# Performance work log

Measured on AMD Instinct MI355X. Metric: run time of the kernel, lower is better.

Reference implementation:

```python
import jax, jax.numpy as jnp
from jax import lax
import numpy as np

B, C, H, W = 8, 256, 64, 64
DSTATE, DCONV, EXPAND = 16, 4, 2
DI = EXPAND * C          # 512 d_inner
DTR = (C + 15) // 16     # 16 dt_rank = ceil(d_model/16)

# ---------- helpers ----------

def _ln(x, g, b):
    m = x.mean(-1, keepdims=True)
    v = x.var(-1, keepdims=True)
    return (x - m) * lax.rsqrt(v + 1e-5) * g + b


def _bn(x, g, b):  # BatchNorm2d, training-mode batch stats
    m = x.mean((0, 2, 3), keepdims=True)
    v = x.var((0, 2, 3), keepdims=True)
    return (x - m) * lax.rsqrt(v + 1e-5) * g[None, :, None, None] + b[None, :, None, None]


def _gn(x, g, b, groups=32):
    Bb, Cc, Hh, Ww = x.shape
    xr = x.reshape(Bb, groups, Cc // groups, Hh, Ww)
    m = xr.mean((2, 3, 4), keepdims=True)
    v = xr.var((2, 3, 4), keepdims=True)
    xr = (xr - m) * lax.rsqrt(v + 1e-5)
    return xr.reshape(Bb, Cc, Hh, Ww) * g[None, :, None, None] + b[None, :, None, None]


def _hsig(x):  # h_sigmoid: relu6(x+3)/6
    return jnp.clip(x + 3.0, 0.0, 6.0) / 6.0


def _axial(v, idx, pos):
    # v: [B,C,N]; pos: [1,C,16] linearly resized to N (align_corners=False == half-pixel)
    N = v.shape[-1]
    pe = jax.image.resize(pos, (1, pos.shape[1], N), method='linear')
    return v + pe + idx  # idx interpolation is identity (same size)


def _dwconvT(x, w):
    # ConvTranspose2d(k=3, stride=2, pad=1, out_pad=1, groups=C) == lhs-dilated corr with flipped kernel
    wf = w[:, :, ::-1, ::-1]
    return lax.conv_general_dilated(x, wf, window_strides=(1, 1), padding=((1, 2), (1, 2)),
                                    lhs_dilation=(2, 2), dimension_numbers=('NCHW', 'OIHW', 'NCHW'),
                                    feature_group_count=x.shape[1])


def _mamba(h, in_w, conv_w, conv_b, xproj_w, dt_w, dt_b, Alog, Dp, out_w):
    # standard mamba_ssm Mamba block forward; h: [B,L,d_model]
    Bb, L, _ = h.shape
    di = in_w.shape[0] // 2
    N = Alog.shape[1]
    dtr = dt_w.shape[1]
    xz = h @ in_w.T                      # [B,L,2*di]
    xm, zg = xz[..., :di], xz[..., di:]
    # causal depthwise conv1d (pad K-1 left == torch pad both + slice [:L])
    xc = lax.conv_general_dilated(xm.transpose(0, 2, 1), conv_w, (1,), [(conv_w.shape[2] - 1, 0)],
                                  dimension_numbers=('NCH', 'OIH', 'NCH'), feature_group_count=di)
    u = jax.nn.silu(xc + conv_b[None, :, None]).transpose(0, 2, 1)  # [B,L,di]
    dbl = u @ xproj_w.T                  # [B,L,dtr+2N]
    dt = jax.nn.softplus(dbl[..., :dtr] @ dt_w.T + dt_b)            # [B,L,di]
    Bm = dbl[..., dtr:dtr + N]
    Cm = dbl[..., dtr + N:]
    A = -jnp.exp(Alog)                   # [di,N]
    dA = jnp.exp(dt[..., None] * A)      # [B,L,di,N]
    dBu = (dt * u)[..., None] * Bm[:, :, None, :]

    def step(hst, inp):
        dA_t, dBu_t = inp
        hst = dA_t * hst + dBu_t
        return hst, hst

    h0 = jnp.zeros((Bb, di, N), dt.dtype)
    _, hs = lax.scan(step, h0, (dA.transpose(1, 0, 2, 3), dBu.transpose(1, 0, 2, 3)))
    y = jnp.einsum('lbdn,bln->bld', hs, Cm) + Dp * u
    y = y * jax.nn.silu(zg)
    return y @ out_w.T


def _forward(x, pos_embed, ln_w, ln_b, proj_w, proj_b,
             up_dw_w, up_bn1_g, up_bn1_b, up_pw_w, up_bn2_g, up_bn2_b,
             down_pw_w, down_bn_g, down_bn_b, gn_g, gn_b,
             f_in_w, f_conv_w, f_conv_b, f_xproj_w, f_dt_w, f_dt_b, f_Alog, f_D, f_out_w,
             b_in_w, b_conv_w, b_conv_b, b_xproj_w, b_dt_w, b_dt_b, b_Alog, b_D, b_out_w):
    # upsample branch: dwconvT -> BN -> ReLU -> 1x1 -> BN -> ReLU6
    z = _dwconvT(x, up_dw_w)
    z = jax.nn.relu(_bn(z, up_bn1_g, up_bn1_b))
    z = jnp.einsum('oc,bchw->bohw', up_pw_w, z)
    z = jnp.clip(_bn(z, up_bn2_g, up_bn2_b), 0.0, 6.0)  # act1 = ReLU6
    dt = x.dtype
    col_max = _ln(_axial(x.max(2), jnp.argmax(x, 2).astype(dt), pos_embed).transpose(0, 2, 1), ln_w, ln_b)
    col_min = _ln(_axial(x.min(2), jnp.argmin(x, 2).astype(dt), pos_embed).transpose(0, 2, 1), ln_w, ln_b)
    row_max = _ln(_axial(x.max(3), jnp.argmax(x, 3).astype(dt), pos_embed).transpose(0, 2, 1), ln_w, ln_b)
    row_min = _ln(_axial(x.min(3), jnp.argmin(x, 3).astype(dt), pos_embed).transpose(0, 2, 1), ln_w, ln_b)
    result_max = jnp.concatenate([col_max, row_max], 1)  # [B, W+H, C]
    result_min = jnp.concatenate([col_min, row_min], 1)
    fpar = (f_in_w, f_conv_w, f_conv_b, f_xproj_w, f_dt_w, f_dt_b, f_Alog, f_D, f_out_w)
    bpar = (b_in_w, b_conv_w, b_conv_b, b_xproj_w, b_dt_w, b_dt_b, b_Alog, b_D, b_out_w)
    fmax = _ln(_mamba(result_max, *fpar), ln_w, ln_b)
    fmin = _ln(_mamba(result_min, *fpar), ln_w, ln_b)
    bmax = _ln(_mamba(jnp.flip(result_max, 1), *bpar), ln_w, ln_b)
    bmin = _ln(_mamba(jnp.flip(result_min, 1), *bpar), ln_w, ln_b)
    res_max = jnp.concatenate([fmax, jnp.flip(bmax, 1)], -1) @ proj_w.T + proj_b
    res_max = _ln(res_max, ln_w, ln_b)
    res_min = jnp.concatenate([fmin, jnp.flip(bmin, 1)], -1) @ proj_w.T + proj_b
    res_min = _ln(res_min, ln_w, ln_b)
    res = res_max[:, :, None, :] + res_min[:, None, :, :]  # [B,L,L,C], L=H+W
    res = res.transpose(0, 3, 1, 2)                        # [B,C,L,L] == [B,C,2H,2W]
    res = _hsig(res) * z
    res = _gn(res, gn_g, gn_b)
    res = jnp.einsum('oc,bchw->bohw', down_pw_w, res[:, :, ::2, ::2])  # 1x1 stride-2 conv
    res = _bn(res, down_bn_g, down_bn_b)
    res = _gn(res, gn_g, gn_b)
    res = res + x
    res = _gn(res, gn_g, gn_b)
    return res


def setup_inputs() -> dict:
    key = jax.random.key(0)
    ks = jax.random.split(key, 32)

    def n(i, shape, s=0.02):
        return jax.random.normal(ks[i], shape, jnp.float32) * s

    inp = {}
    inp['x'] = jax.random.normal(ks[0], (B, C, H, W), jnp.float32)
    inp['pos_embed'] = jax.random.normal(ks[1], (1, C, 16), jnp.float32)
    inp['ln_w'] = jnp.ones((C,), jnp.float32)
    inp['ln_b'] = jnp.zeros((C,), jnp.float32)
    inp['proj_w'] = n(2, (C, 2 * C))
    inp['proj_b'] = jnp.zeros((C,), jnp.float32)
    inp['up_dw_w'] = n(3, (C, 1, 3, 3), 0.1)
    inp['up_bn1_g'] = jnp.ones((C,), jnp.float32)
    inp['up_bn1_b'] = jnp.zeros((C,), jnp.float32)
    inp['up_pw_w'] = n(4, (C, C), 0.05)
    inp['up_bn2_g'] = jnp.ones((C,), jnp.float32)
    inp['up_bn2_b'] = jnp.zeros((C,), jnp.float32)
    inp['down_pw_w'] = n(5, (C, C), 0.05)
    inp['down_bn_g'] = jnp.ones((C,), jnp.float32)
    inp['down_bn_b'] = jnp.zeros((C,), jnp.float32)
    inp['gn_g'] = jnp.ones((C,), jnp.float32)
    inp['gn_b'] = jnp.zeros((C,), jnp.float32)
    Alog = jnp.tile(jnp.log(jnp.arange(1, DSTATE + 1, dtype=jnp.float32))[None, :], (DI, 1))
    dtb = jnp.full((DI,), float(np.log(np.expm1(0.01))), jnp.float32)
    for p, k0 in (('f', 6), ('b', 16)):
        inp[p + '_in_w'] = n(k0, (2 * DI, C))
        inp[p + '_conv_w'] = n(k0 + 1, (DI, 1, DCONV), 0.2)
        inp[p + '_conv_b'] = jnp.zeros((DI,), jnp.float32)
        inp[p + '_xproj_w'] = n(k0 + 2, (DTR + 2 * DSTATE, DI))
        inp[p + '_dt_w'] = n(k0 + 3, (DI, DTR), 0.1)
        inp[p + '_dt_b'] = dtb
        inp[p + '_Alog'] = Alog
        inp[p + '_D'] = jnp.ones((DI,), jnp.float32)
        inp[p + '_out_w'] = n(k0 + 4, (C, DI))
    return inp


def reference(x, pos_embed, ln_w, ln_b, proj_w, proj_b,
              up_dw_w, up_bn1_g, up_bn1_b, up_pw_w, up_bn2_g, up_bn2_b,
              down_pw_w, down_bn_g, down_bn_b, gn_g, gn_b,
              f_in_w, f_conv_w, f_conv_b, f_xproj_w, f_dt_w, f_dt_b, f_Alog, f_D, f_out_w,
              b_in_w, b_conv_w, b_conv_b, b_xproj_w, b_dt_w, b_dt_b, b_Alog, b_D, b_out_w):
    return _forward(x, pos_embed, ln_w, ln_b, proj_w, proj_b,
                    up_dw_w, up_bn1_g, up_bn1_b, up_pw_w, up_bn2_g, up_bn2_b,
                    down_pw_w, down_bn_g, down_bn_b, gn_g, gn_b,
                    f_in_w, f_conv_w, f_conv_b, f_xproj_w, f_dt_w, f_dt_b, f_Alog, f_D, f_out_w,
                    b_in_w, b_conv_w, b_conv_b, b_xproj_w, b_dt_w, b_dt_b, b_Alog, b_D, b_out_w)
```

## Files before the change

### kernel.cpp

```cpp
#include <hip/hip_runtime.h>
#include <hip/hip_bf16.h>

typedef __hip_bfloat16 bf16;
typedef __attribute__((ext_vector_type(8))) short bf16x8v;
typedef __attribute__((ext_vector_type(4))) short bf16x4v;
typedef __attribute__((ext_vector_type(4))) float f32x4v;

#define B_ 8
#define C_ 256
#define L_ 128
#define MB 1048576UL

__device__ inline float b2f(bf16 v){ return __bfloat162float(v); }
__device__ inline bf16 f2b(float v){ return __float2bfloat16(v); }
__device__ inline float siluf(float x){ return x / (1.f + expf(-x)); }
__device__ inline float softplusf(float x){ return (x > 20.f) ? x : log1pf(expf(x)); }
__device__ inline float vclamp(float v){ return fmaxf(v, 0.f) + 1e-5f; }

__device__ inline void bred2(float& a, float& b, float* red){
  int t = threadIdx.x;
  __syncthreads();
  red[t] = a; red[256 + t] = b;
  __syncthreads();
  for (int off = 128; off > 0; off >>= 1){
// ... 22 lines not shown
  if (tt <= 0.f) pe = pp[0];
  else if (tt >= 15.f) pe = pp[15];
  else { int f = (int)floorf(tt); float w = tt - (float)f; pe = pp[f]*(1.f - w) + pp[f+1]*w; }
  float vmax = -1e30f, vmin = 1e30f; int amax = 0, amin = 0;
  for (int j = 0; j < 64; j++){
    float v = xs[t][j];
    if (v > vmax){ vmax = v; amax = j; }
    if (v < vmin){ vmin = v; amin = j; }
  }
  long o = (long)(b*64 + t)*C_ + c;
  prowmax[o] = vmax + pe + (float)amax;
  prowmin[o] = vmin + pe + (float)amin;
  vmax = -1e30f; vmin = 1e30f; amax = 0; amin = 0;
  float sx = 0.f, sx2 = 0.f;
  for (int i = 0; i < 64; i++){
    float v = xs[i][t];
    if (v > vmax){ vmax = v; amax = i; }
    if (v < vmin){ vmin = v; amin = i; }
    sx += v; sx2 += v*v;
  }
  pcolmax[o] = vmax + pe + (float)amax;
  pcolmin[o] = vmin + pe + (float)amin;
  #pragma unroll
  for (int m = 1; m < 64; m <<= 1){ sx += __shfl_xor(sx, m); sx2 += __shfl_xor(sx2, m); }
  if (t == 0){ sxb[(b << 8) + c] = sx; sxb[2048 + (b << 8) + c] = sx2; }
}

__global__ __launch_bounds__(256) void pool2_kernel(const float* __restrict__ pcolmax, const float* __restrict__ pcolmin,
    const float* __restrict__ prowmax, const float* __restrict__ prowmin,
    const float* __restrict__ lnw, const float* __restrict__ lnb, bf16* __restrict__ hbuf)
{
  int r = blockIdx.x, b = blockIdx.y, c = threadIdx.x;
  __shared__ float red[512];
  int p = r & 63;
  long src = (long)(b*64 + p)*C_ + c;
  float vmax = (r < 64) ? pcolmax[src] : prowmax[src];
  float vmin = (r < 64) ? pcolmin[src] : prowmin[src];
  float gw = lnw[c], gb = lnb[c];
  long row = (long)b*L_ + r, frow = (long)b*L_ + (127 - r);
  float s = vmax, s2 = vmax*vmax;
  bred2(s, s2, red);
  float m = s*(1.f/256.f), var = s2*(1.f/256.f) - m*m;
  float o = (vmax - m)*rsqrtf(vclamp(var))*gw + gb;
  hbuf[0*262144 + row*C_ + c]  = f2b(o);
  hbuf[2*262144 + frow*C_ + c] = f2b(o);
  s = vmin; s2 = vmin*vmin;
  bred2(s, s2, red);
  m = s*(1.f/256.f); var = s2*(1.f/256.f) - m*m;
  o = (vmin - m)*rsqrtf(vclamp(var))*gw + gb;
  hbuf[1*262144 + row*C_ + c]  = f2b(o);
  hbuf[3*262144 + frow*C_ + c] = f2b(o);
}

__device__ inline float dwconvT_at(const float* __restrict__ xp, const float* __restrict__ w, int i, int j)
{
  float acc = 0.f;
  #pragma unroll
  for (int ki = 0; ki < 3; ki++){
    int pi = i + ki - 1;
    if (pi < 0 || (pi & 1)) continue;
    int xi = pi >> 1;
    if (xi >= 64) continue;
    #pragma unroll
    for (int kj = 0; kj < 3; kj++){
      int pj = j + kj - 1;
      if (pj < 0 || (pj & 1)) continue;
      int xj = pj >> 1;
      if (xj >= 64) continue;
      acc += w[(2-ki)*3 + (2-kj)] * xp[xi*64 + xj];
    }
  }
  return acc;
}

__global__ __launch_bounds__(256) void dwz1_kernel(const float* __restrict__ x, const float* __restrict__ dw,
    bf16* __restrict__ z1, float* __restrict__ bn1sum, float* __restrict__ bn1sq)
{
  int bc = blockIdx.x; int c = bc & 255;
  int tid = threadIdx.x;
  __shared__ float xs[4096];
  const float* xp = x + (long)bc*4096;
  for (int it = 0; it < 16; it++) xs[it*256 + tid] = xp[it*256 + tid];
  float w[9];
  #pragma unroll
  for (int q = 0; q < 9; q++) w[q] = dw[c*9 + q];
  __syncthreads();
  bf16* zp = z1 + (long)bc*16384;
  float s = 0.f, s2 = 0.f;
  for (int it = 0; it < 64; it++){
    int p = it*256 + tid; int i = p >> 7, j = p & 127;
    float acc = dwconvT_at(xs, w, i, j);
    zp[p] = f2b(acc);
    s += acc; s2 += acc*acc;
  }
  __shared__ float red[512];
  bred2(s, s2, red);
  if (tid == 0){ atomicAdd(&bn1sum[c], s); atomicAdd(&bn1sq[c], s2); }
}

__global__ void fin_bn_kernel(const float* __restrict__ sum, const float* __restrict__ sq,
                              const float* __restrict__ g, const float* __restrict__ b,
                              float cnt_inv, float* __restrict__ a, float* __restrict__ d)
{
  int c = threadIdx.x;
  float m = sum[c]*cnt_inv;
  float v = sq[c]*cnt_inv - m*m;
  float aa = g[c] * rsqrtf(vclamp(v));
  a[c] = aa;
  d[c] = b[c] - m*aa;
}

__global__ void fin_bn2_kernel(const float* __restrict__ part,
                               const float* __restrict__ g, const float* __restrict__ b,
                               float* __restrict__ a, float* __restrict__ d)
{
  int c = threadIdx.x;
  float s = 0.f, s2 = 0.f;
  for (int k = 0; k < 64; k++){ s += part[k*256 + c]; s2 += part[16384 + k*256 + c]; }
  float m = s*(1.f/131072.f);
  float v = s2*(1.f/131072.f) - m*m;
  float aa = g[c] * rsqrtf(vclamp(v));
  a[c] = aa;
  d[c] = b[c] - m*aa;
}

__global__ __launch_bounds__(256) void wcvt_all_kernel(
    const float* __restrict__ s0, const float* __restrict__ s1, const float* __restrict__ s2,
    const float* __restrict__ s3, const float* __restrict__ s4, const float* __restrict__ s5,
    const float* __restrict__ s6, const float* __restrict__ s7, const float* __restrict__ s8,
    bf16* __restrict__ d0, bf16* __restrict__ d1, bf16* __restrict__ d2,
    bf16* __restrict__ d3, bf16* __restrict__ d4, bf16* __restrict__ d5,
    bf16* __restrict__ d6, bf16* __restrict__ d7, bf16* __restrict__ d8)
{
  int seg = blockIdx.y;
  const float* s; bf16* d; int n;
  switch (seg){
    case 0: s = s0; d = d0; n = 262144; break;
    case 1: s = s1; d = d1; n = 262144; break;
    case 2: s = s2; d = d2; n = 24576;  break;
    case 3: s = s3; d = d3; n = 24576;  break;
    case 4: s = s4; d = d4; n = 131072; break;
    case 5: s = s5; d = d5; n = 131072; break;
    case 6: s = s6; d = d6; n = 131072; break;
    case 7: s = s7; d = d7; n = 65536;  break;
    default: s = s8; d = d8; n = 65536; break;
  }
  long i = ((long)blockIdx.x*256 + threadIdx.x)*4;
  if (i >= n) return;
  float4 v = *(const float4*)&s[i];
  bf16 o[4] = {f2b(v.x), f2b(v.y), f2b(v.z), f2b(v.w)};
  *(uint2*)&d[i] = *(const uint2*)o;
}

__global__ __launch_bounds__(256) void pwz_fused_kernel(const bf16* __restrict__ z1,
    const float* __restrict__ fa, const float* __restrict__ fd,
    const bf16* __restrict__ Wb, bf16* __restrict__ z2,
    float* __restrict__ bn2part)
{
  int b = blockIdx.y;
  int p0 = blockIdx.x*64;
  int tid = threadIdx.x;
  __shared__ __align__(16) short Tb[16384];
  {
    int pc = tid & 15, ch = tid >> 4;
    #pragma unroll
    for (int it = 0; it < 8; it++){
      int c2 = ch + it*16;
      int c = c2*2;
      const bf16* r0 = &z1[((long)(b*C_ + c))*16384 + p0 + pc*4];
      bf16x4v va = *(const bf16x4v*)r0;
      bf16x4v vb = *(const bf16x4v*)(r0 + 16384);
      float a0 = fa[c], d0 = fd[c], a1 = fa[c+1], d1 = fd[c+1];
      #pragma unroll
      for (int k = 0; k < 4; k++){
        int p = pc*4 + k;
        bf16 h0; *(short*)&h0 = va[k];
        bf16 h1; *(short*)&h1 = vb[k];
        bf16 o0 = f2b(fmaxf(b2f(h0)*a0 + d0, 0.f));
        bf16 o1 = f2b(fmaxf(b2f(h1)*a1 + d1, 0.f));
        unsigned int u = ((unsigned int)(*(unsigned short*)&o1) << 16) | (unsigned int)(*(unsigned short*)&o0);
        *(unsigned int*)((char*)Tb + tswz(p, c)) = u;
      }
    }
  }
  __syncthreads();
  int wave = tid >> 6, lane = tid & 63;
  int quad = lane >> 4, l16 = lane & 15;
  f32x4v acc[4][4];
  #pragma unroll
  for (int i = 0; i < 4; i++)
    #pragma unroll
    for (int j = 0; j < 4; j++) acc[i][j] = (f32x4v){0.f, 0.f, 0.f, 0.f};
  for (int k0 = 0; k0 < 256; k0 += 32){
    int c = k0 + quad*8;
    bf16x8v a[4], bb[4];
    #pragma unroll
    for (int ms = 0; ms < 4; ms++)
      a[ms] = *(const bf16x8v*)&Wb[(wave*64 + ms*16 + l16)*C_ + c];
    #pragma unroll
    for (int ns = 0; ns < 4; ns++){
      int p = ns*16 + l16;
      bb[ns] = *(const bf16x8v*)((const char*)Tb + tswz(p, c));
    }
    #pragma unroll
    for (int ms = 0; ms < 4; ms++)
      #pragma unroll
      for (int ns = 0; ns < 4; ns++)
        acc[ms][ns] = __builtin_amdgcn_mfma_f32_16x16x32_bf16(a[ms], bb[ns], acc[ms][ns], 0, 0, 0);
  }
  int slot = (blockIdx.x & 7) | (b << 3);
  #pragma unroll
  for (int ms = 0; ms < 4; ms++){
    int o = wave*64 + ms*16 + quad*4;
    #pragma unroll
    for (int r = 0; r < 4; r++){
      long rowbase = ((long)(b*C_ + o + r))*16384 + p0;
      float s = 0.f, s2 = 0.f;
      #pragma unroll
      for (int ns = 0; ns < 4; ns++){
        bf16 bv = f2b(acc[ms][ns][r]);
        z2[rowbase + ns*16 + l16] = bv;
        float vv = b2f(bv);
        s += vv; s2 += vv*vv;
      }
      #pragma unroll
      for (int m = 1; m < 16; m <<= 1){ s += __shfl_xor(s, m); s2 += __shfl_xor(s2, m); }
      if (l16 == 0){
        atomicAdd(&bn2part[slot*256 + o + r], s);
        atomicAdd(&bn2part[16384 + slot*256 + o + r], s2);
      }
    }
  }
}

__global__ __launch_bounds__(256) void inproj_mfma_kernel(const bf16* __restrict__ hb,
    const bf16* __restrict__ Wif, const bf16* __restrict__ Wib2, bf16* __restrict__ xz)
{
  int v = blockIdx.z;
  int m0 = blockIdx.y*256, n0 = blockIdx.x*64;
  const bf16* A = hb + (long)v*262144;
  const bf16* W = (v >= 2) ? Wib2 : Wif;
  bf16* out = xz + (long)v*1048576;
  int tid = threadIdx.x;
  int wave = tid >> 6, lane = tid & 63;
  int quad = lane >> 4, l16 = lane & 15;
  f32x4v acc[4][4];
  #pragma unroll
  for (int i = 0; i < 4; i++)
    #pragma unroll
    for (int j = 0; j < 4; j++) acc[i][j] = (f32x4v){0.f, 0.f, 0.f, 0.f};
  for (int k0 = 0; k0 < 256; k0 += 32){
    int c = k0 + quad*8;
    bf16x8v a[4], bb[4];
    #pragma unroll
    for (int ms = 0; ms < 4; ms++)
      a[ms] = *(const bf16x8v*)&A[(long)(m0 + wave*64 + ms*16 + l16)*256 + c];
    #pragma unroll
    for (int ns = 0; ns < 4; ns++)
      bb[ns] = *(const bf16x8v*)&W[(long)(n0 + ns*16 + l16)*256 + c];
    #pragma unroll
    for (int ms = 0; ms < 4; ms++)
      #pragma unroll
      for (int ns = 0; ns < 4; ns++)
        acc[ms][ns] = __builtin_amdgcn_mfma_f32_16x16x32_bf16(a[ms], bb[ns], acc[ms][ns], 0, 0, 0);
  }
  #pragma unroll
  for (int ms = 0; ms < 4; ms++){
    int m = m0 + wave*64 + ms*16 + quad*4;
    #pragma unroll
    for (int r = 0; r < 4; r++){
      long rowbase = (long)(m + r)*1024 + n0;
      #pragma unroll
      for (int ns = 0; ns < 4; ns++)
        out[rowbase + ns*16 + l16] = f2b(acc[ms][ns][r]);
    }
  }
}

__global__ __launch_bounds__(256) void xproj_mfma_kernel(const bf16* __restrict__ ub,
    const bf16* __restrict__ Wxf, const bf16* __restrict__ Wxb, float* __restrict__ dblb)
{
  int v = blockIdx.y;
  int m0 = blockIdx.x*256;
  const bf16* A = ub + (long)v*524288;
  const bf16* W = (v >= 2) ? Wxb : Wxf;
// ... 235 lines not shown
  float Dv = Dp[d];
  float h[4];
  #pragma unroll
  for (int n = 0; n < 4; n++) h[n] = 0.f;
  __syncthreads();
  bf16* yo = yb + (long)v*1024*512;
  for (int l = 0; l < 128; l++){
    float dtv = b2f(sdt[l*16 + dd]);
    float uv  = b2f(su [l*16 + dd]);
    float zgv = b2f(szg[l*16 + dd]);
    bf16x4v Bv = *(const bf16x4v*)&sbc[l*32 + qtr*4];
    bf16x4v Cv = *(const bf16x4v*)&sbc[l*32 + 16 + qtr*4];
    float dtu = dtv*uv;
    float acc = 0.f;
    #pragma unroll
    for (int n = 0; n < 4; n++){
      float dA = exp2f(dtv*a2[n]);
      bf16 tb; *(short*)&tb = Bv[n];
      bf16 tc; *(short*)&tc = Cv[n];
      h[n] = dA*h[n] + dtu*b2f(tb);
      acc += h[n]*b2f(tc);
    }
    acc += __shfl_xor(acc, 16);
    acc += __shfl_xor(acc, 32);
    if (qtr == 0)
      yo[(row + l)*512 + d] = f2b((acc + Dv*uv) * siluf(zgv));
  }
}

__global__ __launch_bounds__(256) void ln_kernel(const float* __restrict__ inb, bf16* __restrict__ outb0,
    bf16* __restrict__ outb1, float* __restrict__ outf,
    const float* __restrict__ lnw, const float* __restrict__ lnb, int mode)
{
  int r = blockIdx.x, b = blockIdx.y, v = blockIdx.z, c = threadIdx.x;
  long row = (long)b*L_ + r;
  float val = inb[((long)v*1024 + row)*C_ + c];
  __shared__ float red[512];
  float s = val, s2 = val*val;
  bred2(s, s2, red);
  float m = s*(1.f/256.f), var = s2*(1.f/256.f) - m*m;
  float o = (val - m)*rsqrtf(vclamp(var))*lnw[c] + lnb[c];
  if (mode == 1){
    long frow = (long)b*L_ + (127 - r);
    if (v == 0)      outb0[row*512 + c] = f2b(o);
    else if (v == 1) outb1[row*512 + c] = f2b(o);
    else if (v == 2) outb0[frow*512 + 256 + c] = f2b(o);
    else             outb1[frow*512 + 256 + c] = f2b(o);
  } else {
    outf[((long)v*1024 + row)*C_ + c] = o;
  }
}

__global__ __launch_bounds__(256) void hsig_kernel(bf16* __restrict__ z2, const float* __restrict__ rm,
    const float* __restrict__ rn, const float* __restrict__ a2, const float* __restrict__ d2,
    float* __restrict__ gnsum, float* __restrict__ gnsq)
{
  int c = blockIdx.x, b = blockIdx.y, tid = threadIdx.x;
  __shared__ float rms[128], rns[128];
  if (tid < 128){
    rms[tid] = rm[(long)(b*L_ + tid)*C_ + c];
    rns[tid] = rn[(long)(b*L_ + tid)*C_ + c];
  }
  __syncthreads();
  float aa = a2[c], dd = d2[c];
  bf16* zp = z2 + ((long)(b*C_ + c))*16384;
  float s = 0.f, s2 = 0.f;
  for (int g = 0; g < 16; g++){
    float tv[4]; int wq[4];
    #pragma unroll
    for (int q = 0; q < 4; q++){
      int p = g*1024 + q*256 + tid; int i = p >> 7, j = p & 127;
      float zv = b2f(zp[p])*aa + dd;
      zv = fminf(fmaxf(zv, 0.f), 6.f);
      float gate = rms[i] + rns[j];
      gate = fminf(fmaxf(gate + 3.f, 0.f), 6.f) * (1.f/6.f);
      float t = gate*zv;
      s += t; s2 += t*t;
      tv[q] = t;
      wq[q] = (((i | j) & 1) == 0) ? ((i >> 1)*64 + (j >> 1)) : -1;
    }
    __syncthreads();
    #pragma unroll
    for (int q = 0; q < 4; q++)
      if (wq[q] >= 0) zp[wq[q]] = f2b(tv[q]);
  }
  __shared__ float red[512];
  bred2(s, s2, red);
  if (tid == 0){ atomicAdd(&gnsum[b*32 + (c >> 3)], s); atomicAdd(&gnsq[b*32 + (c >> 3)], s2); }
}

__global__ void fin_gn_kernel(const float* __restrict__ gnsum, const float* __restrict__ gnsq,
                              const float* __restrict__ g, const float* __restrict__ bb,
                              float* __restrict__ gnA, float* __restrict__ gnD)
{
  int b = blockIdx.x, c = threadIdx.x, gr = c >> 3;
  float inv_cnt = 1.f/131072.f;
  float m = gnsum[b*32 + gr]*inv_cnt;
  float v = gnsq[b*32 + gr]*inv_cnt - m*m;
  float inv = rsqrtf(vclamp(v));
  float A = inv*g[c];
  gnA[b*C_ + c] = A;
  gnD[b*C_ + c] = bb[c] - m*A;
}

__global__ __launch_bounds__(256) void pwdown_fused_kernel(const bf16* __restrict__ z2,
    const float* __restrict__ gnA, const float* __restrict__ gnD,
    const bf16* __restrict__ Wb, const float* __restrict__ x,
    float* __restrict__ out, float* __restrict__ sds)
{
  int b = blockIdx.y;
  int p0 = blockIdx.x*64;
  int tid = threadIdx.x;
  __shared__ __align__(16) short Tb[16384];
  {
    int pc = tid & 15, ch = tid >> 4;
    #pragma unroll
    for (int it = 0; it < 8; it++){
      int c2 = ch + it*16;
      int c = c2*2;
      const bf16* r0 = &z2[((long)(b*C_ + c))*16384 + p0 + pc*4];
      bf16x4v va = *(const bf16x4v*)r0;
      bf16x4v vb = *(const bf16x4v*)(r0 + 16384);
      float a0 = gnA[b*C_ + c], d0 = gnD[b*C_ + c];
      float a1 = gnA[b*C_ + c + 1], d1 = gnD[b*C_ + c + 1];
      #pragma unroll
      for (int k = 0; k < 4; k++){
        int p = pc*4 + k;
        bf16 h0; *(short*)&h0 = va[k];
        bf16 h1; *(short*)&h1 = vb[k];
        bf16 o0 = f2b(b2f(h0)*a0 + d0);
        bf16 o1 = f2b(b2f(h1)*a1 + d1);
        unsigned int u = ((unsigned int)(*(unsigned short*)&o1) << 16) | (unsigned int)(*(unsigned short*)&o0);
        *(unsigned int*)((char*)Tb + tswz(p, c)) = u;
      }
    }
  }
  __syncthreads();
  int wave = tid >> 6, lane = tid & 63;
  int quad = lane >> 4, l16 = lane & 15;
  f32x4v acc[4][4];
  #pragma unroll
  for (int i = 0; i < 4; i++)
    #pragma unroll
    for (int j = 0; j < 4; j++) acc[i][j] = (f32x4v){0.f, 0.f, 0.f, 0.f};
  for (int k0 = 0; k0 < 256; k0 += 32){
    int c = k0 + quad*8;
    bf16x8v a[4], bb[4];
    #pragma unroll
    for (int ms = 0; ms < 4; ms++)
      a[ms] = *(const bf16x8v*)&Wb[(wave*64 + ms*16 + l16)*C_ + c];
    #pragma unroll
    for (int ns = 0; ns < 4; ns++){
      int p = ns*16 + l16;
      bb[ns] = *(const bf16x8v*)((const char*)Tb + tswz(p, c));
    }
    #pragma unroll
    for (int ms = 0; ms < 4; ms++)
      #pragma unroll
      for (int ns = 0; ns < 4; ns++)
        acc[ms][ns] = __builtin_amdgcn_mfma_f32_16x16x32_bf16(a[ms], bb[ns], acc[ms][ns], 0, 0, 0);
  }
  #pragma unroll
  for (int ms = 0; ms < 4; ms++){
    int o = wave*64 + ms*16 + quad*4;
    #pragma unroll
    for (int r = 0; r < 4; r++){
      long rowbase = ((long)(b*C_ + o + r))*4096 + p0;
      float sd = 0.f, sd2 = 0.f, sdx = 0.f;
      #pragma unroll
      for (int ns = 0; ns < 4; ns++){
        float v = acc[ms][ns][r];
        out[rowbase + ns*16 + l16] = v;
        float xv = x[rowbase + ns*16 + l16];
        sd += v; sd2 += v*v; sdx += v*xv;
      }
      #pragma unroll
      for (int m = 1; m < 16; m <<= 1){
        sd += __shfl_xor(sd, m); sd2 += __shfl_xor(sd2, m); sdx += __shfl_xor(sdx, m);
      }
      if (l16 == 0){
        int oc = (b << 8) + o + r;
        atomicAdd(&sds[oc], sd);
        atomicAdd(&sds[2048 + oc], sd2);
        atomicAdd(&sds[4096 + oc], sdx);
      }
    }
  }
}

__global__ void coeff_kernel(const float* __restrict__ sds, const float* __restrict__ sxb,
                             const float* __restrict__ dbn_g, const float* __restrict__ dbn_b,
                             const float* __restrict__ gn_g, const float* __restrict__ gn_b, float* __restrict__ pqr)
{
  int b = blockIdx.x, c = threadIdx.x, g = c >> 3;
  float sd = 0, sd2 = 0;
  for (int bb = 0; bb < 8; bb++){ sd += sds[bb*256 + c]; sd2 += sds[2048 + bb*256 + c]; }
  float inv_cnt = 1.f/32768.f;
  float mB = sd*inv_cnt;
  float vB = sd2*inv_cnt - mB*mB;
  float ab = dbn_g[c] * rsqrtf(vclamp(vB));
  float db = dbn_b[c] - mB*ab;
  float inv_n = 1.f/4096.f;
  float m = sds[b*256 + c]*inv_n, Ed2 = sds[2048 + b*256 + c]*inv_n;
  float mx = sxb[b*256 + c]*inv_n, Ex2 = sxb[2048 + b*256 + c]*inv_n;
  float Edx = sds[4096 + b*256 + c]*inv_n;
  float Ev = ab*m + db;
  float Ev2 = ab*ab*Ed2 + 2.f*ab*db*m + db*db;
  __shared__ float e1[256], e2[256];
  e1[c] = Ev; e2[c] = Ev2;
  __syncthreads();
  float m1 = 0, q1 = 0;
  for (int k = 0; k < 8; k++){ m1 += e1[(g << 3) + k]; q1 += e2[(g << 3) + k]; }
  m1 *= 0.125f; q1 *= 0.125f;
  float inv1 = rsqrtf(vclamp(q1 - m1*m1));
  float gg = gn_g[c];
  float A1 = inv1*gg;
  float D1 = gn_b[c] - m1*A1;
  float al = A1*ab;
  float be = A1*db + D1;
  float Et = al*m + be + mx;
  float Et2 = al*al*Ed2 + 2.f*al*be*m + be*be + 2.f*al*Edx + 2.f*be*mx + Ex2;
  __syncthreads();
  e1[c] = Et; e2[c] = Et2;
  __syncthreads();
  float m2 = 0, q2 = 0;
  for (int k = 0; k < 8; k++){ m2 += e1[(g << 3) + k]; q2 += e2[(g << 3) + k]; }
  m2 *= 0.125f; q2 *= 0.125f;
  float inv2 = rsqrtf(vclamp(q2 - m2*m2));
  float G = inv2*gg;
  float* o = pqr + (long)(b*C_ + c)*3;
  o[0] = G*al;
  o[1] = G;
  o[2] = G*(be - m2) + gn_b[c];
}

__global__ __launch_bounds__(256) void final_kernel(const float* __restrict__ x,
    const float* __restrict__ pqr, float* __restrict__ out)
{
  int c = blockIdx.x, b = blockIdx.y, tid = threadIdx.x;
  const float* o = pqr + (long)(b*C_ + c)*3;
  float P = o[0], Q = o[1], R = o[2];
  long base = ((long)(b*C_ + c))*4096;
  for (int it = 0; it < 16; it++){
    long idx = base + it*256 + tid;
    out[idx] = P*out[idx] + Q*x[idx] + R;
  }
}

extern "C" void kernel_launch(void* const* d_in, const int* in_sizes, int n_in,
                              void* d_out, int out_size, void* d_ws, size_t ws_size,
                              hipStream_t stream)
{
  (void)in_sizes; (void)n_in; (void)out_size; (void)ws_size;
  const float* x         = (const float*)d_in[0];
  const float* pos       = (const float*)d_in[1];
  const float* ln_w      = (const float*)d_in[2];
  const float* ln_b      = (const float*)d_in[3];
  const float* proj_w    = (const float*)d_in[4];
  const float* proj_b    = (const float*)d_in[5];
  const float* up_dw_w   = (const float*)d_in[6];
  const float* up_bn1_g  = (const float*)d_in[7];
  const float* up_bn1_b  = (const float*)d_in[8];
  const float* up_pw_w   = (const float*)d_in[9];
  const float* up_bn2_g  = (const float*)d_in[10];
  const float* up_bn2_b  = (const float*)d_in[11];
  const float* down_pw_w = (const float*)d_in[12];
  const float* down_bn_g = (const float*)d_in[13];
  const float* down_bn_b = (const float*)d_in[14];
  const float* gn_g      = (const float*)d_in[15];
  const float* gn_b      = (const float*)d_in[16];
  const float* f_in_w    = (const float*)d_in[17];
  const float* f_conv_w  = (const float*)d_in[18];
  const float* f_conv_b  = (const float*)d_in[19];
  const float* f_xproj_w = (const float*)d_in[20];
  const float* f_dt_w    = (const float*)d_in[21];
  const float* f_dt_b    = (const float*)d_in[22];
  const float* f_Alog    = (const float*)d_in[23];
  const float* f_D       = (const float*)d_in[24];
  const float* f_out_w   = (const float*)d_in[25];
  const float* b_in_w    = (const float*)d_in[26];
  const float* b_conv_w  = (const float*)d_in[27];
  const float* b_conv_b  = (const float*)d_in[28];
  const float* b_xproj_w = (const float*)d_in[29];
  const float* b_dt_w    = (const float*)d_in[30];
  const float* b_dt_b    = (const float*)d_in[31];
  const float* b_Alog    = (const float*)d_in[32];
  const float* b_D       = (const float*)d_in[33];
  const float* b_out_w   = (const float*)d_in[34];

  char* sb = (char*)d_ws;
  float* statz  = (float*)(sb);
  float* sds    = (float*)(sb + 6144);
  float* bn2part= (float*)(sb + 32768);
  float* abn    = (float*)(sb + 163840);
  float* gnAD   = (float*)(sb + 167936);
  float* sxb    = (float*)(sb + 184320);
  float* pqr    = (float*)(sb + 200704);
  float* rmrn  = (float*)(sb + 1*MB);
  bf16*  Wbbuf = (bf16*)(sb + 3*MB);
  bf16*  Wb2buf= (bf16*)(sb + 3*MB + 262144);
  bf16*  Wpb   = (bf16*)(sb + 3*MB + 524288);
  char* big = sb + 4*MB;
  float* pool4  = (float*)(big + 0*MB);
  bf16*  hbufb  = (bf16*)(big + 2*MB);
  bf16*  Wif    = (bf16*)(big + 4*MB);
  bf16*  Wib2   = (bf16*)(big + 4*MB + 524288);
  bf16*  Wxf    = (bf16*)(big + 5*MB);
  bf16*  Wxb    = (bf16*)(big + 5*MB + 65536);
  bf16*  Wof    = (bf16*)(big + 5*MB + 131072);
  bf16*  Wob    = (bf16*)(big + 5*MB + 393216);
  bf16*  xzbuf  = (bf16*)(big + 6*MB);
  bf16*  ubuf   = (bf16*)(big + 22*MB);
  float* dblbuf = (float*)(big + 30*MB);
  float* dtbuf  = (float*)(big + 31*MB);
  bf16*  ybuf   = (bf16*)(big + 39*MB);
  float* mout   = (float*)(big + 47*MB);
  bf16*  cbufb  = (bf16*)(big + 51*MB);
  float* respre = (float*)(big + 55*MB);
  bf16*  z1buf  = (bf16*)(big);
  bf16*  z2buf  = (bf16*)(big);
  float* dbuf   = (float*)d_out;

  float* bn1sum = statz;        float* bn1sq = statz + 256;
  float* gnsum  = statz + 1024; float* gnsq  = statz + 1280;
  float* abn1 = abn;       float* dbn1 = abn + 256;
  float* abn2 = abn + 512; float* dbn2 = abn + 768;
  float* gnA = gnAD;       float* gnD = gnAD + 2048;
  float* pcolmax = pool4;
  float* pcolmin = pool4 + 131072;
  float* prowmax = pool4 + 262144;
  float* prowmin = pool4 + 393216;

  hipMemsetAsync(statz, 0, 163840, stream);

  wcvt_all_kernel<<<dim3(256, 9), 256, 0, stream>>>(
      f_in_w, b_in_w, f_xproj_w, b_xproj_w, f_out_w, b_out_w, proj_w, up_pw_w, down_pw_w,
      Wif, Wib2, Wxf, Wxb, Wof, Wob, Wpb, Wbbuf, Wb2buf);

  pool1_kernel<<<dim3(256, 8), 64, 0, stream>>>(x, pos, pcolmax, pcolmin, prowmax, prowmin, sxb);
  pool2_kernel<<<dim3(128, 8), 256, 0, stream>>>(pcolmax, pcolmin, prowmax, prowmin, ln_w, ln_b, hbufb);
  inproj_mfma_kernel<<<dim3(16, 4, 4), 256, 0, stream>>>(hbufb, Wif, Wib2, xzbuf);
  conv1d_kernel<<<dim3(128, 8, 4), 512, 0, stream>>>(xzbuf, f_conv_w, f_conv_b, b_conv_w, b_conv_b, ubuf);
  xproj_mfma_kernel<<<dim3(4, 4), 256, 0, stream>>>(ubuf, Wxf, Wxb, dblbuf);
  gemm_kernel<<<dim3(8, 16, 4), 256, 0, stream>>>(dblbuf, 49152, 48, f_dt_w, b_dt_w, f_dt_b, b_dt_b, 2,
                                                  dtbuf, 524288, 512, 1024, 512, 16, 2);
  scan_kernel<<<dim3(32, 8, 4), 64, 0, stream>>>(dtbuf, ubuf, dblbuf, xzbuf, f_Alog, f_D, b_Alog, b_D, ybuf);
  outproj_mfma_kernel<<<dim3(4, 4, 4), 256, 0, stream>>>(ybuf, Wof, Wob, mout);
  ln_kernel<<<dim3(128, 8, 4), 256, 0, stream>>>(mout, cbufb, cbufb + 524288, nullptr, ln_w, ln_b, 1);
  pj_mfma_kernel<<<dim3(4, 4, 2), 256, 0, stream>>>(cbufb, Wpb, proj_b, respre);
  ln_kernel<<<dim3(128, 8, 2), 256, 0, stream>>>(respre, nullptr, nullptr, rmrn, ln_w, ln_b, 0);

  dwz1_kernel<<<2048, 256, 0, stream>>>(x, up_dw_w, z1buf, bn1sum, bn1sq);
  fin_bn_kernel<<<1, 256, 0, stream>>>(bn1sum, bn1sq, up_bn1_g, up_bn1_b, 1.f/131072.f, abn1, dbn1);
  pwz_fused_kernel<<<dim3(256, 8), 256, 0, stream>>>(z1buf, abn1, dbn1, Wbbuf, z2buf, bn2part);
  fin_bn2_kernel<<<1, 256, 0, stream>>>(bn2part, up_bn2_g, up_bn2_b, abn2, dbn2);

  hsig_kernel<<<dim3(256, 8), 256, 0, stream>>>(z2buf, rmrn, rmrn + 262144, abn2, dbn2, gnsum, gnsq);
  fin_gn_kernel<<<8, 256, 0, stream>>>(gnsum, gnsq, gn_g, gn_b, gnA, gnD);
  pwdown_fused_kernel<<<dim3(64, 8), 256, 0, stream>>>(z2buf, gnA, gnD, Wb2buf, x, dbuf, sds);
  coeff_kernel<<<8, 256, 0, stream>>>(sds, sxb, down_bn_g, down_bn_b, gn_g, gn_b, pqr);
  final_kernel<<<dim3(256, 8), 256, 0, stream>>>(x, pqr, (float*)d_out);
}
```

Measured before the change: 514.3 us.

## Fold stat-finalize kernels into consumers and prefetch second tile in pwz

Removes four tiny finalize launches (fin_bn, fin_bn2, fin_gn, coeff) by recomputing the BN/GN scale and shift inside the consuming kernels (pwz, hsig, pwdown, final). pwz_fused now handles two 64-pixel tiles per block, loading the second tile into registers while the first GEMM runs. The transposed depthwise conv is rewritten as a branch-free four-tap gather. This cuts launch and serialization overhead in exchange for redundant per-block statistics math and higher register and LDS use in pwz.

New measurement: 512.0 us. No clear change (-0.5%).

```diff
diff --git a/kernel.cpp b/kernel.cpp
--- a/kernel.cpp
+++ b/kernel.cpp
@@ -98,27 +98,6 @@
   hbuf[3*262144 + frow*C_ + c] = f2b(o);
 }
 
-__device__ inline float dwconvT_at(const float* __restrict__ xp, const float* __restrict__ w, int i, int j)
-{
-  float acc = 0.f;
-  #pragma unroll
-  for (int ki = 0; ki < 3; ki++){
-    int pi = i + ki - 1;
-    if (pi < 0 || (pi & 1)) continue;
-    int xi = pi >> 1;
-    if (xi >= 64) continue;
-    #pragma unroll
-    for (int kj = 0; kj < 3; kj++){
-      int pj = j + kj - 1;
-      if (pj < 0 || (pj & 1)) continue;
-      int xj = pj >> 1;
-      if (xj >= 64) continue;
-      acc += w[(2-ki)*3 + (2-kj)] * xp[xi*64 + xj];
-    }
-  }
-  return acc;
-}
-
 __global__ __launch_bounds__(256) void dwz1_kernel(const float* __restrict__ x, const float* __restrict__ dw,
     bf16* __restrict__ z1, float* __restrict__ bn1sum, float* __restrict__ bn1sq)
 {
@@ -135,39 +114,28 @@
   float s = 0.f, s2 = 0.f;
   for (int it = 0; it < 64; it++){
     int p = it*256 + tid; int i = p >> 7, j = p & 127;
-    float acc = dwconvT_at(xs, w, i, j);
+    int xi = i >> 1, xj = j >> 1;
+    int io = i & 1, jo = j & 1;
+    int xi1 = (xi < 63) ? xi + 1 : 63;
+    int xj1 = (xj < 63) ? xj + 1 : 63;
+    float XA = xs[xi*64 + xj];
+    float XB = xs[xi*64 + xj1];
+    float XC = xs[xi1*64 + xj];
+    float XD = xs[xi1*64 + xj1];
+    float wA = jo ? (io ? w[8] : w[5]) : (io ? w[7] : w[4]);
+    float wB = (jo && j < 127) ? (io ? w[6] : w[3]) : 0.f;
+    float wC = (io && i < 127) ? (jo ? w[2] : w[1]) : 0.f;
+    float wD = (io && jo && i < 127 && j < 127) ? w[0] : 0.f;
+    float acc = wA*XA;
+    acc += wB*XB;
+    acc += wC*XC;
+    acc += wD*XD;
     zp[p] = f2b(acc);
     s += acc; s2 += acc*acc;
   }
   __shared__ float red[512];
   bred2(s, s2, red);
   if (tid == 0){ atomicAdd(&bn1sum[c], s); atomicAdd(&bn1sq[c], s2); }
-}
-
-__global__ void fin_bn_kernel(const float* __restrict__ sum, const float* __restrict__ sq,
-                              const float* __restrict__ g, const float* __restrict__ b,
-                              float cnt_inv, float* __restrict__ a, float* __restrict__ d)
-{
-  int c = threadIdx.x;
-  float m = sum[c]*cnt_inv;
-  float v = sq[c]*cnt_inv - m*m;
-  float aa = g[c] * rsqrtf(vclamp(v));
-  a[c] = aa;
-  d[c] = b[c] - m*aa;
-}
-
-__global__ void fin_bn2_kernel(const float* __restrict__ part,
-                               const float* __restrict__ g, const float* __restrict__ b,
-                               float* __restrict__ a, float* __restrict__ d)
-{
-  int c = threadIdx.x;
-  float s = 0.f, s2 = 0.f;
-  for (int k = 0; k < 64; k++){ s += part[k*256 + c]; s2 += part[16384 + k*256 + c]; }
-  float m = s*(1.f/131072.f);
-  float v = s2*(1.f/131072.f) - m*m;
-  float aa = g[c] * rsqrtf(vclamp(v));
-  a[c] = aa;
-  d[c] = b[c] - m*aa;
 }
 
 __global__ __launch_bounds__(256) void wcvt_all_kernel(
@@ -198,38 +166,10 @@
   *(uint2*)&d[i] = *(const uint2*)o;
 }
 
-__global__ __launch_bounds__(256) void pwz_fused_kernel(const bf16* __restrict__ z1,
-    const float* __restrict__ fa, const float* __restrict__ fd,
-    const bf16* __restrict__ Wb, bf16* __restrict__ z2,
-    float* __restrict__ bn2part)
-{
-  int b = blockIdx.y;
-  int p0 = blockIdx.x*64;
-  int tid = threadIdx.x;
-  __shared__ __align__(16) short Tb[16384];
-  {
-    int pc = tid & 15, ch = tid >> 4;
-    #pragma unroll
-    for (int it = 0; it < 8; it++){
-      int c2 = ch + it*16;
-      int c = c2*2;
-      const bf16* r0 = &z1[((long)(b*C_ + c))*16384 + p0 + pc*4];
-      bf16x4v va = *(const bf16x4v*)r0;
-      bf16x4v vb = *(const bf16x4v*)(r0 + 16384);
-      float a0 = fa[c], d0 = fd[c], a1 = fa[c+1], d1 = fd[c+1];
-      #pragma unroll
-      for (int k = 0; k < 4; k++){
-        int p = pc*4 + k;
-        bf16 h0; *(short*)&h0 = va[k];
-        bf16 h1; *(short*)&h1 = vb[k];
-        bf16 o0 = f2b(fmaxf(b2f(h0)*a0 + d0, 0.f));
-        bf16 o1 = f2b(fmaxf(b2f(h1)*a1 + d1, 0.f));
-        unsigned int u = ((unsigned int)(*(unsigned short*)&o1) << 16) | (unsigned int)(*(unsigned short*)&o0);
-        *(unsigned int*)((char*)Tb + tswz(p, c)) = u;
-      }
-    }
-  }
-  __syncthreads();
+__device__ inline void pwz_gemm_tile(const short* __restrict__ Tbh, const bf16* __restrict__ Wb,
+    bf16* __restrict__ z2, float* __restrict__ bn2part,
+    int b, int pbase, int slot, int tid)
+{
   int wave = tid >> 6, lane = tid & 63;
   int quad = lane >> 4, l16 = lane & 15;
   f32x4v acc[4][4];
@@ -246,7 +186,7 @@
     #pragma unroll
     for (int ns = 0; ns < 4; ns++){
       int p = ns*16 + l16;
-      bb[ns] = *(const bf16x8v*)((const char*)Tb + tswz(p, c));
+      bb[ns] = *(const bf16x8v*)((const char*)Tbh + tswz(p, c));
     }
     #pragma unroll
     for (int ms = 0; ms < 4; ms++)
@@ -254,13 +194,12 @@
       for (int ns = 0; ns < 4; ns++)
         acc[ms][ns] = __builtin_amdgcn_mfma_f32_16x16x32_bf16(a[ms], bb[ns], acc[ms][ns], 0, 0, 0);
   }
-  int slot = (blockIdx.x & 7) | (b << 3);
   #pragma unroll
   for (int ms = 0; ms < 4; ms++){
     int o = wave*64 + ms*16 + quad*4;
     #pragma unroll
     for (int r = 0; r < 4; r++){
-      long rowbase = ((long)(b*C_ + o + r))*16384 + p0;
+      long rowbase = ((long)(b*C_ + o + r))*16384 + pbase;
       float s = 0.f, s2 = 0.f;
       #pragma unroll
       for (int ns = 0; ns < 4; ns++){
@@ -277,6 +216,73 @@
       }
     }
   }
+}
+
+__global__ __launch_bounds__(256) void pwz_fused_kernel(const bf16* __restrict__ z1,
+    const float* __restrict__ bn1sum, const float* __restrict__ bn1sq,
+    const float* __restrict__ g1, const float* __restrict__ b1,
+    const bf16* __restrict__ Wb, bf16* __restrict__ z2,
+    float* __restrict__ bn2part)
+{
+  int b = blockIdx.y;
+  int p0 = blockIdx.x*128;
+  int tid = threadIdx.x;
+  __shared__ __align__(16) short Tb[2][16384];
+  __shared__ float aa[256], dd[256];
+  {
+    float m = bn1sum[tid]*(1.f/131072.f);
+    float v = bn1sq[tid]*(1.f/131072.f) - m*m;
+    float a = g1[tid]*rsqrtf(vclamp(v));
+    aa[tid] = a; dd[tid] = b1[tid] - m*a;
+  }
+  __syncthreads();
+  int pc = tid & 15, ch = tid >> 4;
+  #pragma unroll
+  for (int it = 0; it < 8; it++){
+    int c = (ch + it*16)*2;
+    const bf16* r0 = &z1[((long)(b*C_ + c))*16384 + p0 + pc*4];
+    bf16x4v va = *(const bf16x4v*)r0;
+    bf16x4v vb = *(const bf16x4v*)(r0 + 16384);
+    float a0 = aa[c], d0 = dd[c], a1 = aa[c+1], d1 = dd[c+1];
+    #pragma unroll
+    for (int k = 0; k < 4; k++){
+      int p = pc*4 + k;
+      bf16 h0; *(short*)&h0 = va[k];
+      bf16 h1; *(short*)&h1 = vb[k];
+      bf16 o0 = f2b(fmaxf(b2f(h0)*a0 + d0, 0.f));
+      bf16 o1 = f2b(fmaxf(b2f(h1)*a1 + d1, 0.f));
+      unsigned int u = ((unsigned int)(*(unsigned short*)&o1) << 16) | (unsigned int)(*(unsigned short*)&o0);
+      *(unsigned int*)((char*)&Tb[0][0] + tswz(p, c)) = u;
+    }
+  }
+  bf16x4v t1a[8], t1b[8];
+  #pragma unroll
+  for (int it = 0; it < 8; it++){
+    int c = (ch + it*16)*2;
+    const bf16* r1 = &z1[((long)(b*C_ + c))*16384 + p0 + 64 + pc*4];
+    t1a[it] = *(const bf16x4v*)r1;
+    t1b[it] = *(const bf16x4v*)(r1 + 16384);
+  }
+  __syncthreads();
+  int slot = (blockIdx.x & 7) | (b << 3);
+  pwz_gemm_tile(&Tb[0][0], Wb, z2, bn2part, b, p0, slot, tid);
+  #pragma unroll
+  for (int it = 0; it < 8; it++){
+    int c = (ch + it*16)*2;
+    float a0 = aa[c], d0 = dd[c], a1 = aa[c+1], d1 = dd[c+1];
+    #pragma unroll
+    for (int k = 0; k < 4; k++){
+      int p = pc*4 + k;
+      bf16 h0; *(short*)&h0 = t1a[it][k];
+      bf16 h1; *(short*)&h1 = t1b[it][k];
+      bf16 o0 = f2b(fmaxf(b2f(h0)*a0 + d0, 0.f));
+      bf16 o1 = f2b(fmaxf(b2f(h1)*a1 + d1, 0.f));
+      unsigned int u = ((unsigned int)(*(unsigned short*)&o1) << 16) | (unsigned int)(*(unsigned short*)&o0);
+      *(unsigned int*)((char*)&Tb[1][0] + tswz(p, c)) = u;
+    }
+  }
+  __syncthreads();
+  pwz_gemm_tile(&Tb[1][0], Wb, z2, bn2part, b, p0 + 64, slot, tid);
 }
 
 __global__ __launch_bounds__(256) void inproj_mfma_kernel(const bf16* __restrict__ hb,
@@ -618,17 +624,25 @@
 }
 
 __global__ __launch_bounds__(256) void hsig_kernel(bf16* __restrict__ z2, const float* __restrict__ rm,
-    const float* __restrict__ rn, const float* __restrict__ a2, const float* __restrict__ d2,
+    const float* __restrict__ rn, const float* __restrict__ bn2part,
+    const float* __restrict__ g2, const float* __restrict__ b2,
     float* __restrict__ gnsum, float* __restrict__ gnsq)
 {
   int c = blockIdx.x, b = blockIdx.y, tid = threadIdx.x;
+  __shared__ float red[512];
+  float pa = 0.f, pb = 0.f;
+  if (tid < 64){ pa = bn2part[tid*256 + c]; pb = bn2part[16384 + tid*256 + c]; }
+  bred2(pa, pb, red);
+  float mm2 = pa*(1.f/131072.f);
+  float vv2 = pb*(1.f/131072.f) - mm2*mm2;
+  float aa = g2[c] * rsqrtf(vclamp(vv2));
+  float dd = b2[c] - mm2*aa;
   __shared__ float rms[128], rns[128];
   if (tid < 128){
     rms[tid] = rm[(long)(b*L_ + tid)*C_ + c];
     rns[tid] = rn[(long)(b*L_ + tid)*C_ + c];
   }
   __syncthreads();
-  float aa = a2[c], dd = d2[c];
   bf16* zp = z2 + ((long)(b*C_ + c))*16384;
   float s = 0.f, s2 = 0.f;
   for (int g = 0; g < 16; g++){
@@ -650,27 +664,13 @@
     for (int q = 0; q < 4; q++)
       if (wq[q] >= 0) zp[wq[q]] = f2b(tv[q]);
   }
-  __shared__ float red[512];
   bred2(s, s2, red);
   if (tid == 0){ atomicAdd(&gnsum[b*32 + (c >> 3)], s); atomicAdd(&gnsq[b*32 + (c >> 3)], s2); }
 }
 
-__global__ void fin_gn_kernel(const float* __restrict__ gnsum, const float* __restrict__ gnsq,
-                              const float* __restrict__ g, const float* __restrict__ bb,
-                              float* __restrict__ gnA, float* __restrict__ gnD)
-{
-  int b = blockIdx.x, c = threadIdx.x, gr = c >> 3;
-  float inv_cnt = 1.f/131072.f;
-  float m = gnsum[b*32 + gr]*inv_cnt;
-  float v = gnsq[b*32 + gr]*inv_cnt - m*m;
-  float inv = rsqrtf(vclamp(v));
-  float A = inv*g[c];
-  gnA[b*C_ + c] = A;
-  gnD[b*C_ + c] = bb[c] - m*A;
-}
-
 __global__ __launch_bounds__(256) void pwdown_fused_kernel(const bf16* __restrict__ z2,
-    const float* __restrict__ gnA, const float* __restrict__ gnD,
+    const float* __restrict__ gnsum, const float* __restrict__ gnsq,
+    const float* __restrict__ gn_g, const float* __restrict__ gn_b,
     const bf16* __restrict__ Wb, const float* __restrict__ x,
     float* __restrict__ out, float* __restrict__ sds)
 {
@@ -678,6 +678,14 @@
   int p0 = blockIdx.x*64;
   int tid = threadIdx.x;
   __shared__ __align__(16) short Tb[16384];
+  __shared__ float gA[256], gD[256];
+  {
+    float m = gnsum[b*32 + (tid >> 3)]*(1.f/131072.f);
+    float v = gnsq[b*32 + (tid >> 3)]*(1.f/131072.f) - m*m;
+    float A = rsqrtf(vclamp(v))*gn_g[tid];
+    gA[tid] = A; gD[tid] = gn_b[tid] - m*A;
+  }
+  __syncthreads();
   {
     int pc = tid & 15, ch = tid >> 4;
     #pragma unroll
@@ -687,8 +695,8 @@
       const bf16* r0 = &z2[((long)(b*C_ + c))*16384 + p0 + pc*4];
       bf16x4v va = *(const bf16x4v*)r0;
       bf16x4v vb = *(const bf16x4v*)(r0 + 16384);
-      float a0 = gnA[b*C_ + c], d0 = gnD[b*C_ + c];
-      float a1 = gnA[b*C_ + c + 1], d1 = gnD[b*C_ + c + 1];
+      float a0 = gA[c], d0 = gD[c];
+      float a1 = gA[c + 1], d1 = gD[c + 1];
       #pragma unroll
       for (int k = 0; k < 4; k++){
         int p = pc*4 + k;
@@ -754,58 +762,57 @@
   }
 }
 
-__global__ void coeff_kernel(const float* __restrict__ sds, const float* __restrict__ sxb,
-                             const float* __restrict__ dbn_g, const float* __restrict__ dbn_b,
-                             const float* __restrict__ gn_g, const float* __restrict__ gn_b, float* __restrict__ pqr)
-{
-  int b = blockIdx.x, c = threadIdx.x, g = c >> 3;
-  float sd = 0, sd2 = 0;
-  for (int bb = 0; bb < 8; bb++){ sd += sds[bb*256 + c]; sd2 += sds[2048 + bb*256 + c]; }
-  float inv_cnt = 1.f/32768.f;
-  float mB = sd*inv_cnt;
-  float vB = sd2*inv_cnt - mB*mB;
-  float ab = dbn_g[c] * rsqrtf(vclamp(vB));
-  float db = dbn_b[c] - mB*ab;
-  float inv_n = 1.f/4096.f;
-  float m = sds[b*256 + c]*inv_n, Ed2 = sds[2048 + b*256 + c]*inv_n;
-  float mx = sxb[b*256 + c]*inv_n, Ex2 = sxb[2048 + b*256 + c]*inv_n;
-  float Edx = sds[4096 + b*256 + c]*inv_n;
-  float Ev = ab*m + db;
-  float Ev2 = ab*ab*Ed2 + 2.f*ab*db*m + db*db;
-  __shared__ float e1[256], e2[256];
-  e1[c] = Ev; e2[c] = Ev2;
-  __syncthreads();
-  float m1 = 0, q1 = 0;
-  for (int k = 0; k < 8; k++){ m1 += e1[(g << 3) + k]; q1 += e2[(g << 3) + k]; }
-  m1 *= 0.125f; q1 *= 0.125f;
-  float inv1 = rsqrtf(vclamp(q1 - m1*m1));
-  float gg = gn_g[c];
-  float A1 = inv1*gg;
-  float D1 = gn_b[c] - m1*A1;
-  float al = A1*ab;
-  float be = A1*db + D1;
-  float Et = al*m + be + mx;
-  float Et2 = al*al*Ed2 + 2.f*al*be*m + be*be + 2.f*al*Edx + 2.f*be*mx + Ex2;
-  __syncthreads();
-  e1[c] = Et; e2[c] = Et2;
-  __syncthreads();
-  float m2 = 0, q2 = 0;
-  for (int k = 0; k < 8; k++){ m2 += e1[(g << 3) + k]; q2 += e2[(g << 3) + k]; }
+__global__ __launch_bounds__(256) void final_kernel(const float* __restrict__ x,
+    const float* __restrict__ sds, const float* __restrict__ sxb,
+    const float* __restrict__ dbn_g, const float* __restrict__ dbn_b,
+    const float* __restrict__ gn_g, const float* __restrict__ gn_b,
+    float* __restrict__ out)
+{
+  int c = blockIdx.x, b = blockIdx.y, tid = threadIdx.x;
+  __shared__ float lv[11][8];
+  int g8 = (c >> 3) << 3;
+  if (tid < 8){
+    int cc = g8 + tid;
+    float sd = 0.f, sd2 = 0.f;
+    for (int bb2 = 0; bb2 < 8; bb2++){ sd += sds[bb2*256 + cc]; sd2 += sds[2048 + bb2*256 + cc]; }
+    float mB = sd*(1.f/32768.f);
+    float vB = sd2*(1.f/32768.f) - mB*mB;
+    float ab = dbn_g[cc] * rsqrtf(vclamp(vB));
+    float db = dbn_b[cc] - mB*ab;
+    float inv_n = 1.f/4096.f;
+    float m = sds[b*256 + cc]*inv_n, Ed2 = sds[2048 + b*256 + cc]*inv_n;
+    float mx = sxb[b*256 + cc]*inv_n, Ex2 = sxb[2048 + b*256 + cc]*inv_n;
+    float Edx = sds[4096 + b*256 + cc]*inv_n;
+    float Ev = ab*m + db;
+    float Ev2 = ab*ab*Ed2 + 2.f*ab*db*m + db*db;
+    lv[0][tid] = ab; lv[1][tid] = db; lv[2][tid] = m; lv[3][tid] = Ed2;
+    lv[4][tid] = mx; lv[5][tid] = Ex2; lv[6][tid] = Edx; lv[7][tid] = Ev; lv[8][tid] = Ev2;
+  }
+  __syncthreads();
+  if (tid < 8){
+    float m1 = 0.f, q1 = 0.f;
+    for (int k = 0; k < 8; k++){ m1 += lv[7][k]; q1 += lv[8][k]; }
+    m1 *= 0.125f; q1 *= 0.125f;
+    int cc = g8 + tid;
+    float inv1 = rsqrtf(vclamp(q1 - m1*m1));
+    float A1 = inv1*gn_g[cc];
+    float D1 = gn_b[cc] - m1*A1;
+    float ab = lv[0][tid], db = lv[1][tid];
+    float m = lv[2][tid], Ed2 = lv[3][tid], mx = lv[4][tid], Ex2 = lv[5][tid], Edx = lv[6][tid];
+    float al = A1*ab;
+    float be = A1*db + D1;
+    float Et = al*m + be + mx;
+    float Et2 = al*al*Ed2 + 2.f*al*be*m + be*be + 2.f*al*Edx + 2.f*be*mx + Ex2;
+    lv[9][tid] = Et; lv[10][tid] = Et2; lv[0][tid] = al; lv[1][tid] = be;
+  }
+  __syncthreads();
+  float m2 = 0.f, q2 = 0.f;
+  for (int k = 0; k < 8; k++){ m2 += lv[9][k]; q2 += lv[10][k]; }
   m2 *= 0.125f; q2 *= 0.125f;
-  float inv2 = rsqrtf(vclamp(q2 - m2*m2));
-  float G = inv2*gg;
-  float* o = pqr + (long)(b*C_ + c)*3;
-  o[0] = G*al;
-  o[1] = G;
-  o[2] = G*(be - m2) + gn_b[c];
-}
-
-__global__ __launch_bounds__(256) void final_kernel(const float* __restrict__ x,
-    const float* __restrict__ pqr, float* __restrict__ out)
-{
-  int c = blockIdx.x, b = blockIdx.y, tid = threadIdx.x;
-  const float* o = pqr + (long)(b*C_ + c)*3;
-  float P = o[0], Q = o[1], R = o[2];
+  float G = rsqrtf(vclamp(q2 - m2*m2))*gn_g[c];
+  float P = G*lv[0][c & 7];
+  float Q = G;
+  float R = G*(lv[1][c & 7] - m2) + gn_b[c];
   long base = ((long)(b*C_ + c))*4096;
   for (int it = 0; it < 16; it++){
     long idx = base + it*256 + tid;
@@ -858,10 +865,7 @@
   float* statz  = (float*)(sb);
   float* sds    = (float*)(sb + 6144);
   float* bn2part= (float*)(sb + 32768);
-  float* abn    = (float*)(sb + 163840);
-  float* gnAD   = (float*)(sb + 167936);
   float* sxb    = (float*)(sb + 184320);
-  float* pqr    = (float*)(sb + 200704);
   float* rmrn  = (float*)(sb + 1*MB);
   bf16*  Wbbuf = (bf16*)(sb + 3*MB);
   bf16*  Wb2buf= (bf16*)(sb + 3*MB + 262144);
@@ -889,9 +893,6 @@
 
   float* bn1sum = statz;        float* bn1sq = statz + 256;
   float* gnsum  = statz + 1024; float* gnsq  = statz + 1280;
-  float* abn1 = abn;       float* dbn1 = abn + 256;
-  float* abn2 = abn + 512; float* dbn2 = abn + 768;
-  float* gnA = gnAD;       float* gnD = gnAD + 2048;
   float* pcolmax = pool4;
   float* pcolmin = pool4 + 131072;
   float* prowmax = pool4 + 262144;
@@ -917,13 +918,13 @@
   ln_kernel<<<dim3(128, 8, 2), 256, 0, stream>>>(respre, nullptr, nullptr, rmrn, ln_w, ln_b, 0);
 
   dwz1_kernel<<<2048, 256, 0, stream>>>(x, up_dw_w, z1buf, bn1sum, bn1sq);
-  fin_bn_kernel<<<1, 256, 0, stream>>>(bn1sum, bn1sq, up_bn1_g, up_bn1_b, 1.f/131072.f, abn1, dbn1);
-  pwz_fused_kernel<<<dim3(256, 8), 256, 0, stream>>>(z1buf, abn1, dbn1, Wbbuf, z2buf, bn2part);
-  fin_bn2_kernel<<<1, 256, 0, stream>>>(bn2part, up_bn2_g, up_bn2_b, abn2, dbn2);
-
-  hsig_kernel<<<dim3(256, 8), 256, 0, stream>>>(z2buf, rmrn, rmrn + 262144, abn2, dbn2, gnsum, gnsq);
-  fin_gn_kernel<<<8, 256, 0, stream>>>(gnsum, gnsq, gn_g, gn_b, gnA, gnD);
-  pwdown_fused_kernel<<<dim3(64, 8), 256, 0, stream>>>(z2buf, gnA, gnD, Wb2buf, x, dbuf, sds);
-  coeff_kernel<<<8, 256, 0, stream>>>(sds, sxb, down_bn_g, down_bn_b, gn_g, gn_b, pqr);
-  final_kernel<<<dim3(256, 8), 256, 0, stream>>>(x, pqr, (float*)d_out);
-}
+  pwz_fused_kernel<<<dim3(128, 8), 256, 0, stream>>>(z1buf, bn1sum, bn1sq, up_bn1_g, up_bn1_b,
+                                                     Wbbuf, z2buf, bn2part);
+
+  hsig_kernel<<<dim3(256, 8), 256, 0, stream>>>(z2buf, rmrn, rmrn + 262144, bn2part,
+                                                up_bn2_g, up_bn2_b, gnsum, gnsq);
+  pwdown_fused_kernel<<<dim3(64, 8), 256, 0, stream>>>(z2buf, gnsum, gnsq, gn_g, gn_b,
+                                                       Wb2buf, x, dbuf, sds);
+  final_kernel<<<dim3(256, 8), 256, 0, stream>>>(x, sds, sxb, down_bn_g, down_bn_b, gn_g, gn_b,
+                                                 (float*)d_out);
+}
```
